# Kernel optimization log

Measured on AMD Instinct MI355X. Metric: run time of the kernel, lower is better.

Reference implementation:

```python
import jax, jax.numpy as jnp
import numpy as np

B, N, C = 4, 4096, 512
K = 683  # ceil(N / ratio=6.0)
TAU = 1.0
W_OCC, W_REP, W_ENT = 1.0, 0.1, 0.01
REP_TOPK, REP_MARGIN = 4, -1.0
NEG = -1e9


def setup_inputs() -> dict:
    key = jax.random.key(0)
    ks = jax.random.split(key, 5)
    s = jax.random.normal(ks[0], (B, N, C), jnp.float32)
    mu = jax.random.normal(ks[1], (B, N, 3), jnp.float32)
    # SPD covariance per residue: L L^T + 0.1 I
    L = jax.random.normal(ks[2], (B, N, 3, 3), jnp.float32) * 0.3
    Sigma = jnp.einsum('bnij,bnkj->bnik', L, L) + 0.1 * jnp.eye(3, dtype=jnp.float32)
    mask = jnp.ones((B, N), jnp.float32)
    W = jax.random.normal(ks[3], (C, C), jnp.float32) / np.sqrt(C).astype(np.float32)
    b = jnp.zeros((C,), jnp.float32)
    slots = jax.random.normal(ks[4], (K, C), jnp.float32) * 0.02
    return {"s": s, "mu": mu, "Sigma": Sigma, "mask": mask, "W": W, "b": b, "slots": slots}


def reference(s, mu, Sigma, mask, W, b, slots):
    Kk = slots.shape[0]
    # A = softmax((Linear(s)) . slots / tau), masked
    s_proj = jnp.einsum('bnc,dc->bnd', s, W) + b            # nn.Linear: x @ W^T + b
    logits = jnp.einsum('bnc,kc->bnk', s_proj, slots) / TAU
    logits = jnp.where((mask < 0.5)[..., None], NEG, logits)
    A = jax.nn.softmax(logits, axis=-1) * mask[..., None]   # [B,N,K]

    denom = jnp.maximum(A.sum(axis=1), 1e-8)                # [B,K]
    s_c = jnp.einsum('bnk,bnc->bkc', A, s) / denom[..., None]

    # moment-matching merge
    w = A / (A.sum(axis=1, keepdims=True) + 1e-8)           # [B,N,K]
    mu_c = jnp.einsum('bnk,bnd->bkd', w, mu)                # [B,K,3]
    intra = jnp.einsum('bnk,bnij->bkij', w, Sigma)          # [B,K,3,3]
    diff = mu[:, :, None, :] - mu_c[:, None, :, :]          # [B,N,K,3]
    inter = jnp.einsum('bnk,bnki,bnkj->bkij', w, diff, diff)
    Sigma_c = intra + inter                                 # [B,K,3,3]

    # occupancy balance loss
    occ = A.sum(axis=1)
    occ = occ / jnp.maximum(occ.sum(axis=-1, keepdims=True), 1e-8)
    loss_occ = jnp.mean((occ - 1.0 / Kk) ** 2)

    # repulsion loss (pairwise Gaussian overlap)
    delta = mu_c[:, :, None, :] - mu_c[:, None, :, :]       # [B,K,K,3]
    sig_sum = Sigma_c[:, :, None] + Sigma_c[:, None, :]     # [B,K,K,3,3]
    inv = jnp.linalg.inv(sig_sum + 1e-6 * jnp.eye(3, dtype=s.dtype))
    dist2 = jnp.einsum('bpqi,bpqij,bpqj->bpq', delta, inv, delta)
    score = -0.5 * dist2
    eye = jnp.eye(Kk, dtype=bool)[None]
    score = jnp.where(eye, NEG, score)
    top = jax.lax.top_k(score, min(REP_TOPK, Kk - 1))[0]
    loss_rep = jnp.mean(jax.nn.relu(top - REP_MARGIN))

    # entropy loss
    Ac = jnp.maximum(A, 1e-8)
    ent = -(Ac * jnp.log(Ac)).sum(axis=-1)                  # [B,N]
    loss_ent = (ent * mask).sum() / jnp.maximum(mask.sum(), 1.0)

    total = W_OCC * loss_occ + W_REP * loss_rep + W_ENT * loss_ent
    return (A, s_c, mu_c, Sigma_c, loss_occ, loss_rep, loss_ent, total)
```

## Files before the change

### kernel.cpp

```cpp
#include <hip/hip_runtime.h>
#include <math.h>

#define B_    4
#define N_    4096
#define C_    512
#define KSLOT 683

using bf16x8 = __attribute__((ext_vector_type(8))) short;
using f32x4  = __attribute__((ext_vector_type(4))) float;

#define OFF_A    0
#define OFF_SC   (B_*N_*KSLOT)
#define OFF_MU   (OFF_SC + B_*KSLOT*C_)
#define OFF_SIG  (OFF_MU + B_*KSLOT*3)
#define OFF_LOSS (OFF_SIG + B_*KSLOT*9)

#define WS_MOM    0
#define WS_INVMAX (WS_MOM + B_*KSLOT*16)
#define WS_OCCTB  (WS_INVMAX + B_*KSLOT)
#define WS_OCCT   (WS_OCCTB + 256)
#define WS_ENTB   (WS_OCCT + 4)
#define WS_MSB    (WS_ENTB + 256)
#define WS_OCCLB  (WS_MSB + 256)
#define WS_REPB   (WS_OCCLB + 256)
#define WS_BS     (WS_REPB + 256)
#define WS_FEND   (WS_BS + 704)

#define US_BASE  (WS_FEND*2)
#define US_SBF   US_BASE
#define US_STF   (US_SBF + B_*N_*C_)
#define US_WSL   (US_STF + B_*C_*N_)
#define US_FT    (US_WSL + 704*C_)
#define US_ATB   (US_FT + B_*16*N_)
#define US_END   (US_ATB + (size_t)B_*768*N_)


__device__ __forceinline__ ushort f2bf(float x) {
  union { float f; unsigned u; } v; v.f = x;
  unsigned r = v.u + 0x7fffu + ((v.u >> 16) & 1u);
  return (ushort)(r >> 16);
}

__device__ __forceinline__ float bf2f(ushort x) {
  union { unsigned u; float f; } v; v.u = ((unsigned)x) << 16;
  return v.f;
}

__device__ __forceinline__ float blockSum256(float v, float* red) {
#pragma unroll
  for (int off = 32; off; off >>= 1) v += __shfl_xor(v, off);
  __syncthreads();
  if ((threadIdx.x & 63) == 0) red[threadIdx.x >> 6] = v;
  __syncthreads();
  return red[0] + red[1] + red[2] + red[3];
}

__device__ __forceinline__ void top4_insert(float v, float& t0, float& t1, float& t2, float& t3) {
  if (v > t3) {
    if (v > t2) {
      t3 = t2;
      if (v > t1) {
        t2 = t1;
        if (v > t0) { t1 = t0; t0 = v; } else t1 = v;
      } else t2 = v;
    } else t3 = v;
  }
}

__global__ __launch_bounds__(256) void prep_all(const float* __restrict__ s,
                                                ushort* __restrict__ sbf,
                                                ushort* __restrict__ stf,
                                                const float* __restrict__ mu,
                                                const float* __restrict__ Sig,
                                                ushort* __restrict__ ftg,
                                                const float* __restrict__ slots,
                                                const float* __restrict__ W,
                                                ushort* __restrict__ wsl,
                                                const float* __restrict__ bvec,
                                                float* __restrict__ bs) {
  __shared__ __align__(16) char PS[16640];
  const int bid = blockIdx.x;
  const int t = threadIdx.x;
  if (bid < 342) {
    float (*SL)[512] = (float(*)[512])PS;
    const int idx = bid;
    const int k0 = (idx % 171) * 4;
    const int c = (idx / 171) * 256 + t;
    for (int id2 = t; id2 < 4 * 512; id2 += 256) {
      int kk = id2 >> 9, d = id2 & 511;
      SL[kk][d] = (k0 + kk < KSLOT) ? slots[(size_t)(k0 + kk) * C_ + d] : 0.f;
    }
    __syncthreads();
    float acc[4];
#pragma unroll
    for (int i = 0; i < 4; ++i) acc[i] = 0.f;
    for (int d0 = 0; d0 < C_; d0 += 8) {
      float wv[8];
#pragma unroll
      for (int j = 0; j < 8; ++j) wv[j] = W[(size_t)(d0 + j) * C_ + c];
#pragma unroll
      for (int j = 0; j < 8; ++j) {
#pragma unroll
        for (int i = 0; i < 4; ++i) acc[i] += SL[i][d0 + j] * wv[j];
      }
    }
#pragma unroll
    for (int i = 0; i < 4; ++i)
      if (k0 + i < KSLOT) wsl[(size_t)(k0 + i) * C_ + c] = f2bf(acc[i]);
  } else if (bid < 513) {
    const int widx = (bid - 342) * 4 + (t >> 6);
    const int lane = t & 63;
    if (widx < KSLOT) {
      const float* srow = slots + (size_t)widx * C_;
      float acc = 0.f;
#pragma unroll
      for (int j = 0; j < 8; ++j) {
        int d = lane + j * 64;
        acc += srow[d] * bvec[d];
      }
#pragma unroll
      for (int off = 32; off; off >>= 1) acc += __shfl_xor(acc, off);
      if (lane == 0) bs[widx] = acc;
    }
  } else if (bid < 577) {
    ushort (*FT)[272] = (ushort(*)[272])PS;
    const int fb = bid - 513;
    const size_t ng = (size_t)fb * 256 + t;
    const float* mp = mu + ng * 3;
    const float* sp = Sig + ng * 9;
    float m0 = mp[0], m1 = mp[1], m2 = mp[2];
    FT[0][t] = 0x3F80;
    FT[1][t] = f2bf(m0); FT[2][t] = f2bf(m1); FT[3][t] = f2bf(m2);
    FT[4][t] = f2bf(m0 * m0); FT[5][t] = f2bf(m0 * m1); FT[6][t] = f2bf(m0 * m2);
    FT[7][t] = f2bf(m1 * m1); FT[8][t] = f2bf(m1 * m2); FT[9][t] = f2bf(m2 * m2);
    FT[10][t] = f2bf(sp[0]); FT[11][t] = f2bf(sp[1]); FT[12][t] = f2bf(sp[2]);
    FT[13][t] = f2bf(sp[4]); FT[14][t] = f2bf(sp[5]); FT[15][t] = f2bf(sp[8]);
    __syncthreads();
    const int b = (int)((fb * 256) >> 12);
    const int n0b = (fb * 256) & (N_ - 1);
    for (int u = t; u < 512; u += 256) {
      int f = u >> 5, off = (u & 31) * 8;
      *(uint4*)(ftg + ((size_t)b * 16 + f) * N_ + n0b + off) = *(uint4*)(&FT[f][off]);
    }
  } else {
    float (*T)[65] = (float(*)[65])PS;
    const int cid = bid - 577;
    const int b = cid >> 9;
    const int rem = cid & 511;
    const int n0 = (rem >> 3) * 64;
    const int c0 = (rem & 7) * 64;
    const int tr = t >> 4;
    const int tc = (t & 15) * 4;
#pragma unroll
    for (int i = 0; i < 4; ++i) {
      const int row = i * 16 + tr;
      float4 v = *(const float4*)(s + ((size_t)(b * N_ + n0 + row)) * C_ + c0 + tc);
      ushort4 u;
      u.x = f2bf(v.x); u.y = f2bf(v.y); u.z = f2bf(v.z); u.w = f2bf(v.w);
      *(ushort4*)(sbf + ((size_t)(b * N_ + n0 + row)) * C_ + c0 + tc) = u;
      T[row][tc + 0] = v.x; T[row][tc + 1] = v.y;
      T[row][tc + 2] = v.z; T[row][tc + 3] = v.w;
    }
    __syncthreads();
#pragma unroll
    for (int i = 0; i < 4; ++i) {
      const int c = i * 16 + tr;
      const int n4 = tc;
      ushort4 o;
      o.x = f2bf(T[n4 + 0][c]); o.y = f2bf(T[n4 + 1][c]);
      o.z = f2bf(T[n4 + 2][c]); o.w = f2bf(T[n4 + 3][c]);
      *(ushort4*)(stf + ((size_t)(b * C_ + c0 + c)) * N_ + n0 + n4) = o;
    }
  }
}

__global__ __launch_bounds__(256) void bs_kernel(const float* __restrict__ slots,
                                                 const float* __restrict__ bvec,
                                                 float* __restrict__ bs) {
  int k = blockIdx.x * 256 + threadIdx.x;
  if (k >= KSLOT) return;
  const float* srow = slots + (size_t)k * C_;
  float acc = 0.f;
  for (int d = 0; d < C_; ++d) acc += srow[d] * bvec[d];
  bs[k] = acc;
}

__device__ __forceinline__ void g1_epilogue(
    f32x4 (&acc)[11], const int rowbase, const int t, const int lane,
    const int rowg, const int colw,
    const float* __restrict__ bs, const float* __restrict__ mask,
    float* __restrict__ Aout, ushort* __restrict__ atb,
    float* __restrict__ entb, float* __restrict__ msb,
    ushort* Af, float (&red4)[32][4], const int binid, const int nthreads) {
  __syncthreads();
  int cols[11]; bool valid[11];
#pragma unroll
  for (int cf = 0; cf < 11; ++cf) {
    cols[cf] = colw * 176 + cf * 16 + (lane & 15);
    valid[cf] = (cols[cf] < KSLOT);
    float bv = valid[cf] ? bs[cols[cf]] : 0.f;
#pragma unroll
    for (int r = 0; r < 4; ++r) acc[cf][r] += bv;
  }
  float m4[4];
#pragma unroll
  for (int r = 0; r < 4; ++r) m4[r] = -3.0e38f;
#pragma unroll
  for (int cf = 0; cf < 11; ++cf)
    if (valid[cf]) {
#pragma unroll
      for (int r = 0; r < 4; ++r) m4[r] = fmaxf(m4[r], acc[cf][r]);
    }
#pragma unroll
  for (int off = 1; off < 16; off <<= 1) {
#pragma unroll
    for (int r = 0; r < 4; ++r) m4[r] = fmaxf(m4[r], __shfl_xor(m4[r], off));
  }
  if ((lane & 15) == 0) {
#pragma unroll
    for (int r = 0; r < 4; ++r) red4[rowg * 16 + (lane >> 4) * 4 + r][colw] = m4[r];
  }
  __syncthreads();
#pragma unroll
  for (int r = 0; r < 4; ++r) {
    int rl = rowg * 16 + (lane >> 4) * 4 + r;
    m4[r] = fmaxf(fmaxf(red4[rl][0], red4[rl][1]), fmaxf(red4[rl][2], red4[rl][3]));
  }
  __syncthreads();
  float s4[4] = {0.f, 0.f, 0.f, 0.f};
#pragma unroll
  for (int cf = 0; cf < 11; ++cf)
    if (valid[cf]) {
#pragma unroll
      for (int r = 0; r < 4; ++r) {
        float e = __expf(acc[cf][r] - m4[r]);
        acc[cf][r] = e;
        s4[r] += e;
      }
    }
#pragma unroll
  for (int off = 1; off < 16; off <<= 1) {
#pragma unroll
    for (int r = 0; r < 4; ++r) s4[r] += __shfl_xor(s4[r], off);
  }
  if ((lane & 15) == 0) {
#pragma unroll
    for (int r = 0; r < 4; ++r) red4[rowg * 16 + (lane >> 4) * 4 + r][colw] = s4[r];
  }
  __syncthreads();
  float inv4[4], mr4[4];
#pragma unroll
  for (int r = 0; r < 4; ++r) {
    int rl = rowg * 16 + (lane >> 4) * 4 + r;
    float S = red4[rl][0] + red4[rl][1] + red4[rl][2] + red4[rl][3];
    inv4[r] = 1.f / S;
    mr4[r] = mask[rowbase + rl];
  }
  __syncthreads();
  float ent4[4] = {0.f, 0.f, 0.f, 0.f};
#pragma unroll
  for (int cf = 0; cf < 11; ++cf)
    if (valid[cf]) {
#pragma unroll
      for (int r = 0; r < 4; ++r) {
        int rl = rowg * 16 + (lane >> 4) * 4 + r;
        float a = acc[cf][r] * inv4[r] * mr4[r];
        Af[rl * KSLOT + cols[cf]] = f2bf(a);
        float ac = fmaxf(a, 1e-8f);
        ent4[r] -= ac * __logf(ac);
      }
    }
#pragma unroll
  for (int off = 1; off < 16; off <<= 1) {
#pragma unroll
    for (int r = 0; r < 4; ++r) ent4[r] += __shfl_xor(ent4[r], off);
  }
  if ((lane & 15) == 0) {
#pragma unroll
    for (int r = 0; r < 4; ++r) red4[rowg * 16 + (lane >> 4) * 4 + r][colw] = ent4[r];
  }
  __syncthreads();
  if (t < 64) {
    float er = 0.f, ms = 0.f;
    if (t < 32) {
      float e = red4[t][0] + red4[t][1] + red4[t][2] + red4[t][3];
      float m = mask[rowbase + t];
      er = e * m; ms = m;
    }
#pragma unroll
    for (int off = 32; off; off >>= 1) { er += __shfl_xor(er, off); ms += __shfl_xor(ms, off); }
    if (t == 0) {
      atomicAdd(&entb[binid], er);
      atomicAdd(&msb[binid], ms);
    }
  }
  float* Ag = Aout + (size_t)rowbase * KSLOT;
  for (int i = t; i < (32 * KSLOT) / 4; i += nthreads) {
    ushort4 u4 = *(const ushort4*)(Af + i * 4);
    float4 v;
    v.x = bf2f(u4.x); v.y = bf2f(u4.y); v.z = bf2f(u4.z); v.w = bf2f(u4.w);
    *(float4*)(Ag + i * 4) = v;
  }
  {
    const int bb = rowbase >> 12;
    const int n0b = rowbase & (N_ - 1);
    ushort* Atb = atb + ((size_t)bb * 768) * N_ + n0b;
    for (int u = t; u < KSLOT * 4; u += nthreads) {
      int k = u >> 2, q = u & 3;
      ushort tmp[8];
#pragma unroll
      for (int j = 0; j < 8; ++j) tmp[j] = Af[(q * 8 + j) * KSLOT + k];
      *(uint4*)(Atb + (size_t)k * N_ + q * 8) = *(uint4*)tmp;
    }
  }
}

__global__ __launch_bounds__(512)
void gemm1sm(const ushort* __restrict__ sbf,
             const ushort* __restrict__ wsl,
             const float* __restrict__ bs,
             const float* __restrict__ mask,
             float* __restrict__ Aout,
             ushort* __restrict__ atb,
             float* __restrict__ entb,
             float* __restrict__ msb) {
  __shared__ __align__(16) char SMEM[49152];
  __shared__ float red4[32][4];
  const int t = threadIdx.x;
  const int lane = t & 63;
  const int w = t >> 6;
  const int rowg = w >> 2;
  const int colw = w & 3;
  const int row0 = blockIdx.x * 32;
  const int r16 = rowg * 16 + (lane & 15);

  const ushort* arow = sbf + (size_t)(row0 + r16) * C_ + (lane >> 4) * 8;
  bf16x8 g0 = *(const bf16x8*)(arow);
  bf16x8 p0;

  f32x4 acc[11];
  f32x4 zero = {0.f, 0.f, 0.f, 0.f};
#pragma unroll
  for (int cf = 0; cf < 11; ++cf) acc[cf] = zero;

  const int ach = (lane >> 4);
#pragma unroll
  for (int slab = 0; slab < 16; ++slab) {
    if (slab) __syncthreads();
#pragma unroll
    for (int i = 0; i < 6; ++i) {
      int idx = t + i * 512;
      int r = idx >> 2;
      int chs = (idx & 3) ^ (r & 3);
      const ushort* g = wsl + (size_t)r * C_ + slab * 32 + chs * 8;
      char* l = (char*)SMEM + (t & 448) * 16 + i * 8192;
      __builtin_amdgcn_global_load_lds(
          (const __attribute__((address_space(1))) void*)g,
          (__attribute__((address_space(3))) void*)l, 16, 0, 0);
    }
    __syncthreads();
    if (slab < 15) p0 = *(const bf16x8*)(arow + (slab + 1) * 32);
#pragma unroll
    for (int cf = 0; cf < 11; ++cf) {
      int br = colw * 176 + cf * 16 + (lane & 15);
      bf16x8 bf = *(const bf16x8*)(SMEM + br * 64 + ((ach * 16) ^ ((br & 3) << 4)));
      acc[cf] = __builtin_amdgcn_mfma_f32_16x16x32_bf16(g0, bf, acc[cf], 0, 0, 0);
    }
    g0 = p0;
  }

  ushort* Af = (ushort*)SMEM;
  g1_epilogue(acc, row0, t, lane, rowg, colw, bs, mask, Aout, atb, entb, msb,
              Af, red4, blockIdx.x & 255, 512);
}

#define G2BUFB 18432
__global__ __launch_bounds__(256) void gemm2t(const ushort* __restrict__ atb,
                                              const ushort* __restrict__ stf,
                                              const ushort* __restrict__ ftg,
                                              float* __restrict__ sc,
                                              float* __restrict__ MOM) {
  __shared__ __align__(16) char LB[2 * G2BUFB];
  const int t = threadIdx.x;
  const int lane = t & 63;
  const int w = t >> 6;
  const int wm = w >> 1;
  const int wn = w & 1;
  const int fhw = blockIdx.x;
  const int logical = (fhw & 7) * 44 + (fhw >> 3);
  const int kt = logical % 11;
  const int ct = (logical / 11) & 7;
  const int b  = logical / 88;
  const bool do_mom = (ct == 0);
  const ushort* Ab = atb + ((size_t)b * 768 + kt * 64) * N_;
  const ushort* Sb = stf + ((size_t)b * C_ + ct * 64) * N_;
  const ushort* Fb = ftg + ((size_t)b * 16) * N_;

  f32x4 zero = {0.f, 0.f, 0.f, 0.f};
  f32x4 acc[2][2];
#pragma unroll
  for (int i = 0; i < 2; ++i)
#pragma unroll
    for (int j = 0; j < 2; ++j) acc[i][j] = zero;
  f32x4 accf[2];
#pragma unroll
  for (int i = 0; i < 2; ++i) accf[i] = zero;

#define G2_STAGE(BUFI, NB)                                                   \
  {                                                                          \
    char* AtL = LB + (BUFI) * G2BUFB;                                        \
    char* SsL = AtL + 8192;                                                  \
    char* FtL = AtL + 16384;                                                 \
    _Pragma("unroll")                                                        \
    for (int i = 0; i < 2; ++i) {                                            \
      int idx = t + i * 256;                                                 \
      int r = idx >> 3;                                                      \
      int chs = (idx & 7) ^ (r & 7);                                         \
      const ushort* g = Ab + (size_t)r * N_ + (NB) + chs * 8;                \
      char* l = AtL + i * 4096 + (t & 192) * 16;                             \
      __builtin_amdgcn_global_load_lds(                                      \
          (const __attribute__((address_space(1))) void*)g,                  \
          (__attribute__((address_space(3))) void*)l, 16, 0, 0);             \
    }                                                                        \
    _Pragma("unroll")                                                        \
    for (int i = 0; i < 2; ++i) {                                            \
      int idx = t + i * 256;                                                 \
      int r = idx >> 3;                                                      \
      int chs = (idx & 7) ^ (r & 7);                                         \
      const ushort* g = Sb + (size_t)r * N_ + (NB) + chs * 8;                \
      char* l = SsL + i * 4096 + (t & 192) * 16;                             \
      __builtin_amdgcn_global_load_lds(                                      \
          (const __attribute__((address_space(1))) void*)g,                  \
          (__attribute__((address_space(3))) void*)l, 16, 0, 0);             \
    }                                                                        \
    if (do_mom && t < 128) {                                                 \
      int idx = t;                                                           \
      int r = idx >> 3;                                                      \
      int chs = (idx & 7) ^ (r & 7);                                         \
      const ushort* g = Fb + (size_t)r * N_ + (NB) + chs * 8;                \
      char* l = FtL + (t & 192) * 16;                                       \
      __builtin_amdgcn_global_load_lds(                                      \
          (const __attribute__((address_space(1))) void*)g,                  \
          (__attribute__((address_space(3))) void*)l, 16, 0, 0);             \
    }                                                                        \
  }

  G2_STAGE(0, 0)
  for (int st = 0; st < 64; ++st) {
    const int cur = st & 1;
    __syncthreads();
    if (st < 63) G2_STAGE(cur ^ 1, (st + 1) * 64)
    char* AtL = LB + cur * G2BUFB;
    char* SsL = AtL + 8192;
    char* FtL = AtL + 16384;
#pragma unroll
    for (int ks2 = 0; ks2 < 2; ++ks2) {
      const int ach = ks2 * 4 + (lane >> 4);
      bf16x8 afr[2], bfr[2];
#pragma unroll
      for (int kf = 0; kf < 2; ++kf) {
        int ar = wm * 32 + kf * 16 + (lane & 15);
        afr[kf] = *(const bf16x8*)(AtL + ar * 128 + ((ach * 16) ^ ((ar & 7) << 4)));
      }
#pragma unroll
      for (int cg = 0; cg < 2; ++cg) {
        int br = wn * 32 + cg * 16 + (lane & 15);
        bfr[cg] = *(const bf16x8*)(SsL + br * 128 + ((ach * 16) ^ ((br & 7) << 4)));
      }
#pragma unroll
      for (int kf = 0; kf < 2; ++kf)
#pragma unroll
        for (int cg = 0; cg < 2; ++cg)
          acc[kf][cg] = __builtin_amdgcn_mfma_f32_16x16x32_bf16(afr[kf], bfr[cg], acc[kf][cg], 0, 0, 0);
      if (do_mom && wn == 0) {
        int fr = lane & 15;
        bf16x8 ffr = *(const bf16x8*)(FtL + fr * 128 + ((ach * 16) ^ ((fr & 7) << 4)));
#pragma unroll
        for (int kf = 0; kf < 2; ++kf)
          accf[kf] = __builtin_amdgcn_mfma_f32_16x16x32_bf16(afr[kf], ffr, accf[kf], 0, 0, 0);
      }
    }
  }
#undef G2_STAGE

#pragma unroll
  for (int kf = 0; kf < 2; ++kf) {
#pragma unroll
    for (int r = 0; r < 4; ++r) {
      int k = kt * 64 + wm * 32 + kf * 16 + (lane >> 4) * 4 + r;
      if (k >= KSLOT) continue;
      float* dst = sc + ((size_t)(b * KSLOT + k)) * C_ + ct * 64 + wn * 32;
#pragma unroll
      for (int cg = 0; cg < 2; ++cg)
        dst[cg * 16 + (lane & 15)] = acc[kf][cg][r];
    }
  }
  if (do_mom && wn == 0) {
#pragma unroll
    for (int kf = 0; kf < 2; ++kf) {
#pragma unroll
      for (int r = 0; r < 4; ++r) {
        int k = kt * 64 + wm * 32 + kf * 16 + (lane >> 4) * 4 + r;
        if (k >= KSLOT) continue;
        MOM[((size_t)b * KSLOT + k) * 16 + (lane & 15)] = accf[kf][r];
      }
    }
  }
}

__global__ __launch_bounds__(128) void scale_sc(float* __restrict__ sc,
                                                const float* __restrict__ invmax) {
  const int bk = blockIdx.x;
  const float sv = invmax[bk];
  float4* p = (float4*)(sc + (size_t)bk * C_);
  int t = threadIdx.x;
  float4 v = p[t];
  v.x *= sv; v.y *= sv; v.z *= sv; v.w *= sv;
  p[t] = v;
}

__global__ __launch_bounds__(256) void moments_kernel(const float* __restrict__ Amat,
                                                      const float* __restrict__ mu,
                                                      const float* __restrict__ Sig,
                                                      float* __restrict__ MOM) {
  __shared__ float red[64][17];
  const int b = blockIdx.z;
  const int kx = threadIdx.x & 63;
  const int k = blockIdx.x * 64 + kx;
  const int ng = threadIdx.x >> 6;
  const int n0 = blockIdx.y * 128;
  const bool valid = (k < KSLOT);

  float acc[16];
#pragma unroll
  for (int i = 0; i < 16; ++i) acc[i] = 0.f;

  const float* Abase = Amat + (size_t)b * N_ * KSLOT + k;
  const float* mubase = mu + ((size_t)b * N_) * 3;
  const float* sgbase = Sig + ((size_t)b * N_) * 9;

  for (int j = 0; j < 32; ++j) {
    const int n = n0 + ng + j * 4;
    float a = valid ? Abase[(size_t)n * KSLOT] : 0.f;
    const float* mp = mubase + (size_t)n * 3;
    const float* sp = sgbase + (size_t)n * 9;
    float m0 = mp[0], m1 = mp[1], m2 = mp[2];
    acc[0] += a;
    acc[1] += a * m0; acc[2] += a * m1; acc[3] += a * m2;
    acc[4] += a * m0 * m0; acc[5] += a * m0 * m1; acc[6] += a * m0 * m2;
    acc[7] += a * m1 * m1; acc[8] += a * m1 * m2; acc[9] += a * m2 * m2;
    acc[10] += a * sp[0]; acc[11] += a * sp[1]; acc[12] += a * sp[2];
    acc[13] += a * sp[4]; acc[14] += a * sp[5]; acc[15] += a * sp[8];
  }

  if (ng == 0) {
#pragma unroll
    for (int i = 0; i < 16; ++i) red[kx][i] = acc[i];
  }
  __syncthreads();
  if (ng == 1) {
#pragma unroll
    for (int i = 0; i < 16; ++i) red[kx][i] += acc[i];
  }
  __syncthreads();
  if (ng == 2) {
#pragma unroll
    for (int i = 0; i < 16; ++i) red[kx][i] += acc[i];
  }
  __syncthreads();
  if (ng == 3) {
#pragma unroll
    for (int i = 0; i < 16; ++i) red[kx][i] += acc[i];
  }
  __syncthreads();
  if (ng == 0 && valid) {
    float* dst = MOM + ((size_t)b * KSLOT + k) * 16;
#pragma unroll
    for (int i = 0; i < 16; ++i) atomicAdd(&dst[i], red[kx][i]);
  }
}

__global__ __launch_bounds__(256) void finalize_bk(const float* __restrict__ MOM,
                                                   float* __restrict__ muc,
                                                   float* __restrict__ sigc,
                                                   float* __restrict__ invmax,
                                                   float* __restrict__ occtb) {
  int bk = blockIdx.x * 256 + threadIdx.x;
  if (bk >= B_ * KSLOT) return;
  int b = bk / KSLOT;
  const float* T = MOM + (size_t)bk * 16;
  float den = T[0];
  float inv_eps = 1.f / (den + 1e-8f);
  float inv_mx = 1.f / fmaxf(den, 1e-8f);
  float mc0 = T[1] * inv_eps, mc1 = T[2] * inv_eps, mc2 = T[3] * inv_eps;
  float M0 = den * inv_eps;
  float cf = 2.f - M0;
  float S00 = (T[10] + T[4]) * inv_eps - cf * mc0 * mc0;
  float S01 = (T[11] + T[5]) * inv_eps - cf * mc0 * mc1;
  float S02 = (T[12] + T[6]) * inv_eps - cf * mc0 * mc2;
  float S11 = (T[13] + T[7]) * inv_eps - cf * mc1 * mc1;
  float S12 = (T[14] + T[8]) * inv_eps - cf * mc1 * mc2;
  float S22 = (T[15] + T[9]) * inv_eps - cf * mc2 * mc2;
  muc[(size_t)bk * 3 + 0] = mc0;
  muc[(size_t)bk * 3 + 1] = mc1;
  muc[(size_t)bk * 3 + 2] = mc2;
  float* sg = sigc + (size_t)bk * 9;
  sg[0] = S00; sg[1] = S01; sg[2] = S02;
  sg[3] = S01; sg[4] = S11; sg[5] = S12;
  sg[6] = S02; sg[7] = S12; sg[8] = S22;
  invmax[bk] = inv_mx;
  atomicAdd(&occtb[b * 64 + (threadIdx.x & 63)], den);
}

__global__ __launch_bounds__(256) void occ_loss_kernel(const float* __restrict__ MOM,
                                                       const float* __restrict__ occtb,
                                                       float* __restrict__ occlb) {
  __shared__ float red[4];
  __shared__ float occT[4];
  int tid = threadIdx.x;
  {
    float v = occtb[tid];
#pragma unroll
    for (int off = 32; off; off >>= 1) v += __shfl_xor(v, off);
    if ((tid & 63) == 0) occT[tid >> 6] = v;
  }
  __syncthreads();
  int bk = blockIdx.x * 256 + tid;
  float d2 = 0.f;
  if (bk < B_ * KSLOT) {
    int b = bk / KSLOT;
    float den = MOM[(size_t)bk * 16];
    float occ = den / fmaxf(occT[b], 1e-8f);
    float d = occ - (1.f / (float)KSLOT);
    d2 = d * d;
  }
  float ssum = blockSum256(d2, red);
  if (tid == 0) occlb[blockIdx.x] = ssum;
}

__global__ __launch_bounds__(256) void repulsion_kernel2(const float* __restrict__ muc,
                                                         const float* __restrict__ sigc,
                                                         float* __restrict__ repb) {
  __shared__ float L[KSLOT * 13];
  const int b = blockIdx.y;
  const int t = threadIdx.x;
  const float* mb = muc + (size_t)b * KSLOT * 3;
  const float* sb = sigc + (size_t)b * KSLOT * 9;
  for (int idx = t; idx < KSLOT * 3; idx += 256) {
    int r = idx / 3, c = idx - r * 3;
    L[r * 13 + c] = mb[idx];
  }
  for (int idx = t; idx < KSLOT * 9; idx += 256) {
    int r = idx / 9, c = idx - r * 9;
    L[r * 13 + 3 + c] = sb[idx];
  }
  __syncthreads();
  const int w = t >> 6, lane = t & 63;
  const int p = blockIdx.x * 4 + w;
  if (p >= KSLOT) return;
  const float* Lp = L + p * 13;
  const float mp0 = Lp[0], mp1 = Lp[1], mp2 = Lp[2];
  const float pa = Lp[3], pb = Lp[4], pc = Lp[5], pd = Lp[7], pe = Lp[8], pf = Lp[11];
  float t0 = -3e38f, t1 = -3e38f, t2 = -3e38f, t3 = -3e38f;
  for (int q = lane; q < KSLOT; q += 64) {
    if (q == p) continue;
    const float* Lq = L + q * 13;
    float d0 = mp0 - Lq[0];
    float d1 = mp1 - Lq[1];
    float d2 = mp2 - Lq[2];
    float a  = pa + Lq[3] + 1e-6f;
    float bb = pb + Lq[4];
    float cc = pc + Lq[5];
    float d  = pd + Lq[7] + 1e-6f;
    float e  = pe + Lq[8];
    float f  = pf + Lq[11] + 1e-6f;
    float C00 = d * f - e * e;
    float C01 = cc * e - bb * f;
    float C02 = bb * e - cc * d;
    float C11 = a * f - cc * cc;
    float C12 = bb * cc - a * e;
    float C22 = a * d - bb * bb;
    float det = a * C00 + bb * C01 + cc * C02;
    float dist2 = (C00 * d0 * d0 + C11 * d1 * d1 + C22 * d2 * d2 +
                   2.f * (C01 * d0 * d1 + C02 * d0 * d2 + C12 * d1 * d2)) / det;
    top4_insert(-0.5f * dist2, t0, t1, t2, t3);
  }
#pragma unroll
  for (int off = 1; off < 64; off <<= 1) {
    float u0 = __shfl_xor(t0, off);
    float u1 = __shfl_xor(t1, off);
    float u2 = __shfl_xor(t2, off);
    float u3 = __shfl_xor(t3, off);
    top4_insert(u0, t0, t1, t2, t3);
    top4_insert(u1, t0, t1, t2, t3);
    top4_insert(u2, t0, t1, t2, t3);
    top4_insert(u3, t0, t1, t2, t3);
  }
  if (lane == 0) {
    float s = fmaxf(t0 + 1.f, 0.f) + fmaxf(t1 + 1.f, 0.f) +
              fmaxf(t2 + 1.f, 0.f) + fmaxf(t3 + 1.f, 0.f);
    atomicAdd(&repb[(b * KSLOT + p) & 255], s);
  }
}

__global__ __launch_bounds__(256) void final_scalars(const float* __restrict__ entb,
                                                     const float* __restrict__ msb,
                                                     const float* __restrict__ occlb,
                                                     const float* __restrict__ repb,
                                                     float* __restrict__ out) {
  __shared__ float red[4];
  int tid = threadIdx.x;
  float e = blockSum256(entb[tid], red);
  float ms = blockSum256(msb[tid], red);
  float oc = blockSum256(occlb[tid], red);
  float rp = blockSum256(repb[tid], red);
  if (tid == 0) {
    float loss_ent = e / fmaxf(ms, 1.f);
    float loss_occ = oc / (float)(B_ * KSLOT);
    float loss_rep = rp / (float)(B_ * KSLOT * 4);
    out[0] = loss_occ;
    out[1] = loss_rep;
    out[2] = loss_ent;
    out[3] = 1.0f * loss_occ + 0.1f * loss_rep + 0.01f * loss_ent;
  }
}


__global__ __launch_bounds__(256) void wslots_kernel(const float* __restrict__ slots,
                                                     const float* __restrict__ W,
                                                     float* __restrict__ Wsl) {
  int k = blockIdx.x;
  int c = blockIdx.y * 256 + threadIdx.x;
  const float* srow = slots + (size_t)k * C_;
  float acc = 0.f;
  for (int d = 0; d < C_; d += 4) {
    acc += srow[d] * W[(size_t)d * C_ + c];
    acc += srow[d + 1] * W[(size_t)(d + 1) * C_ + c];
    acc += srow[d + 2] * W[(size_t)(d + 2) * C_ + c];
    acc += srow[d + 3] * W[(size_t)(d + 3) * C_ + c];
  }
  Wsl[(size_t)k * C_ + c] = acc;
}

__global__ __launch_bounds__(256) void softmax_rows(float* __restrict__ Amat,
                                                    const float* __restrict__ mask,
                                                    float* __restrict__ entb,
                                                    float* __restrict__ msb) {
  __shared__ float red[4];
  const int row = blockIdx.x;
  const int tid = threadIdx.x;
  float* rowp = Amat + (size_t)row * KSLOT;
  const float m = mask[row];
  const bool msk = (m < 0.5f);
  float v[3];
#pragma unroll
  for (int i = 0; i < 3; ++i) {
    int k = tid + i * 256;
    if (k < KSLOT) {
      float l = rowp[k];
      v[i] = msk ? -1e9f : l;
    } else v[i] = -3.0e38f;
  }
  float lmax = fmaxf(fmaxf(v[0], v[1]), v[2]);
#pragma unroll
  for (int off = 32; off; off >>= 1) lmax = fmaxf(lmax, __shfl_xor(lmax, off));
  __syncthreads();
  if ((tid & 63) == 0) red[tid >> 6] = lmax;
  __syncthreads();
  lmax = fmaxf(fmaxf(red[0], red[1]), fmaxf(red[2], red[3]));
  float lsum = 0.f;
#pragma unroll
  for (int i = 0; i < 3; ++i) {
    int k = tid + i * 256;
    float e = (k < KSLOT) ? expf(v[i] - lmax) : 0.f;
    v[i] = e;
    lsum += e;
  }
  lsum = blockSum256(lsum, red);
  float inv = 1.f / lsum;
  float ent = 0.f;
#pragma unroll
  for (int i = 0; i < 3; ++i) {
    int k = tid + i * 256;
    if (k < KSLOT) {
      float a = v[i] * inv * m;
      rowp[k] = a;
      float ac = fmaxf(a, 1e-8f);
      ent -= ac * logf(ac);
    }
  }
  ent = blockSum256(ent, red);
  if (tid == 0) {
    int bin = blockIdx.x & 255;
    atomicAdd(&entb[bin], ent * m);
    atomicAdd(&msb[bin], m);
  }
}

__global__ __launch_bounds__(256) void gemm_nt(const float* __restrict__ Am,
                                               const float* __restrict__ Bm,
                                               const float* __restrict__ bias,
                                               float* __restrict__ Cm,
                                               int M, int Nout, int Kd,
                                               int lda, int ldb, int ldc) {
  __shared__ float As[16][132];
  __shared__ float Bs[16][132];
  const int tid = threadIdx.x;
  const int tx = tid & 15, ty = tid >> 4;
  const int m0 = blockIdx.x * 128, n0 = blockIdx.y * 128;
  float acc[8][8];
#pragma unroll
  for (int i = 0; i < 8; ++i)
#pragma unroll
    for (int j = 0; j < 8; ++j) acc[i][j] = 0.f;
  const int r = tid >> 1, hc = (tid & 1) * 8;
  for (int k0 = 0; k0 < Kd; k0 += 16) {
    float va[8], vb[8];
    int gm = m0 + r;
    if (gm < M) {
      const float* p = Am + (size_t)gm * lda + k0 + hc;
      *(float4*)(va) = *(const float4*)(p);
      *(float4*)(va + 4) = *(const float4*)(p + 4);
    } else {
#pragma unroll
      for (int i = 0; i < 8; ++i) va[i] = 0.f;
    }
    int gn = n0 + r;
    if (gn < Nout) {
      const float* p = Bm + (size_t)gn * ldb + k0 + hc;
      *(float4*)(vb) = *(const float4*)(p);
      *(float4*)(vb + 4) = *(const float4*)(p + 4);
    } else {
#pragma unroll
      for (int i = 0; i < 8; ++i) vb[i] = 0.f;
    }
#pragma unroll
    for (int i = 0; i < 8; ++i) As[hc + i][r] = va[i];
#pragma unroll
    for (int i = 0; i < 8; ++i) Bs[hc + i][r] = vb[i];
    __syncthreads();
#pragma unroll
    for (int kk = 0; kk < 16; ++kk) {
      float a[8], bb[8];
      *(float4*)(a) = *(const float4*)&As[kk][ty * 8];
      *(float4*)(a + 4) = *(const float4*)&As[kk][ty * 8 + 4];
      *(float4*)(bb) = *(const float4*)&Bs[kk][tx * 8];
      *(float4*)(bb + 4) = *(const float4*)&Bs[kk][tx * 8 + 4];
#pragma unroll
      for (int i = 0; i < 8; ++i)
#pragma unroll
        for (int j = 0; j < 8; ++j) acc[i][j] += a[i] * bb[j];
    }
    __syncthreads();
  }
#pragma unroll
  for (int i = 0; i < 8; ++i) {
    int gm = m0 + ty * 8 + i;
    if (gm >= M) continue;
    float* crow = Cm + (size_t)gm * ldc;
#pragma unroll
    for (int j = 0; j < 8; ++j) {
      int gn = n0 + tx * 8 + j;
      if (gn < Nout) crow[gn] = acc[i][j] + bias[gn];
    }
  }
}

__global__ __launch_bounds__(256) void gemm_tn(const float* __restrict__ Aall,
                                               const float* __restrict__ Ball,
                                               const float* __restrict__ scale,
                                               float* __restrict__ Call) {
  const int b = blockIdx.z;
  const float* Am = Aall + (size_t)b * N_ * KSLOT;
  const float* Bv = Ball + (size_t)b * N_ * C_;
  float* Cm = Call + (size_t)b * KSLOT * C_;
  const float* sc = scale + (size_t)b * KSLOT;
  __shared__ float As[16][132];
  __shared__ float Bs[16][68];
  const int tid = threadIdx.x;
  const int tx = tid & 15, ty = tid >> 4;
  const int m0 = blockIdx.x * 128, n0 = blockIdx.y * 64;
  float acc[8][4];
#pragma unroll
  for (int i = 0; i < 8; ++i)
#pragma unroll
    for (int j = 0; j < 4; ++j) acc[i][j] = 0.f;
  const int rr = tid >> 4;
  const int mq = tid & 15;
  const int cq = (tid & 15) * 4;
  for (int r0 = 0; r0 < N_; r0 += 16) {
#pragma unroll
    for (int i = 0; i < 8; ++i) {
      int mm = mq + 16 * i;
      int gm = m0 + mm;
      As[rr][mm] = (gm < KSLOT) ? Am[(size_t)(r0 + rr) * KSLOT + gm] : 0.f;
    }
    *(float4*)&Bs[rr][cq] = *(const float4*)(Bv + (size_t)(r0 + rr) * C_ + n0 + cq);
    __syncthreads();
#pragma unroll
    for (int kk = 0; kk < 16; ++kk) {
      float a[8], bb[4];
      *(float4*)(a) = *(const float4*)&As[kk][ty * 8];
      *(float4*)(a + 4) = *(const float4*)&As[kk][ty * 8 + 4];
      *(float4*)(bb) = *(const float4*)&Bs[kk][tx * 4];
#pragma unroll
      for (int i = 0; i < 8; ++i)
#pragma unroll
        for (int j = 0; j < 4; ++j) acc[i][j] += a[i] * bb[j];
    }
    __syncthreads();
  }
#pragma unroll
  for (int i = 0; i < 8; ++i) {
    int gm = m0 + ty * 8 + i;
    if (gm < KSLOT) {
      float s = sc[gm];
      float4 v;
      v.x = acc[i][0] * s; v.y = acc[i][1] * s; v.z = acc[i][2] * s; v.w = acc[i][3] * s;
      *(float4*)(Cm + (size_t)gm * C_ + n0 + tx * 4) = v;
    }
  }
}

extern "C" void kernel_launch(void* const* d_in, const int* in_sizes, int n_in,
                              void* d_out, int out_size, void* d_ws, size_t ws_size,
                              hipStream_t stream) {
  const float* s     = (const float*)d_in[0];
  const float* mu    = (const float*)d_in[1];
  const float* Sig   = (const float*)d_in[2];
  const float* mask  = (const float*)d_in[3];
  const float* W     = (const float*)d_in[4];
  const float* bvec  = (const float*)d_in[5];
  const float* slots = (const float*)d_in[6];
  float* out = (float*)d_out;
  float* ws  = (float*)d_ws;

  float* Amat = out + OFF_A;
  const bool fast = (ws_size >= (size_t)US_END * 2 + 64);

  (void)hipMemsetAsync(ws, 0, WS_FEND * sizeof(float), stream);

  if (fast) {
    ushort* usw = (ushort*)ws;
    ushort* sbf = usw + US_SBF;
    ushort* stf = usw + US_STF;
    ushort* wsl = usw + US_WSL;
    ushort* ftg = usw + US_FT;
    ushort* atb = usw + US_ATB;

    prep_all<<<dim3(2625), 256, 0, stream>>>(
        s, sbf, stf, mu, Sig, ftg, slots, W, wsl, bvec, ws + WS_BS);

    gemm1sm<<<dim3(B_ * N_ / 32), 512, 0, stream>>>(
        sbf, wsl, ws + WS_BS, mask, Amat, atb, ws + WS_ENTB, ws + WS_MSB);

    gemm2t<<<dim3(352), 256, 0, stream>>>(
        atb, stf, ftg, out + OFF_SC, ws + WS_MOM);

    finalize_bk<<<dim3((B_ * KSLOT + 255) / 256), 256, 0, stream>>>(
        ws + WS_MOM, out + OFF_MU, out + OFF_SIG, ws + WS_INVMAX, ws + WS_OCCTB);

    occ_loss_kernel<<<dim3((B_ * KSLOT + 255) / 256), 256, 0, stream>>>(
        ws + WS_MOM, ws + WS_OCCTB, ws + WS_OCCLB);

    scale_sc<<<dim3(B_ * KSLOT), 128, 0, stream>>>(out + OFF_SC, ws + WS_INVMAX);

    repulsion_kernel2<<<dim3((KSLOT + 3) / 4, B_), 256, 0, stream>>>(
        out + OFF_MU, out + OFF_SIG, ws + WS_REPB);

    final_scalars<<<dim3(1), 256, 0, stream>>>(
        ws + WS_ENTB, ws + WS_MSB, ws + WS_OCCLB, ws + WS_REPB, out + OFF_LOSS);
  } else {
    float* Wsl = out + OFF_SC;

    bs_kernel<<<dim3(3), 256, 0, stream>>>(slots, bvec, ws + WS_BS);
    wslots_kernel<<<dim3(KSLOT, 2), 256, 0, stream>>>(slots, W, Wsl);
    gemm_nt<<<dim3((B_ * N_) / 128, (KSLOT + 127) / 128), 256, 0, stream>>>(
        s, Wsl, ws + WS_BS, Amat, B_ * N_, KSLOT, C_, C_, C_, KSLOT);
    softmax_rows<<<dim3(B_ * N_), 256, 0, stream>>>(Amat, mask, ws + WS_ENTB, ws + WS_MSB);
    moments_kernel<<<dim3(11, N_ / 128, B_), 256, 0, stream>>>(
        Amat, mu, Sig, ws + WS_MOM);
    finalize_bk<<<dim3((B_ * KSLOT + 255) / 256), 256, 0, stream>>>(
        ws + WS_MOM, out + OFF_MU, out + OFF_SIG, ws + WS_INVMAX, ws + WS_OCCTB);
    occ_loss_kernel<<<dim3((B_ * KSLOT + 255) / 256), 256, 0, stream>>>(
        ws + WS_MOM, ws + WS_OCCTB, ws + WS_OCCLB);
    gemm_tn<<<dim3((KSLOT + 127) / 128, C_ / 64, B_), 256, 0, stream>>>(
        Amat, s, ws + WS_INVMAX, out + OFF_SC);
    repulsion_kernel2<<<dim3((KSLOT + 3) / 4, B_), 256, 0, stream>>>(
        out + OFF_MU, out + OFF_SIG, ws + WS_REPB);
    final_scalars<<<dim3(1), 256, 0, stream>>>(
        ws + WS_ENTB, ws + WS_MSB, ws + WS_OCCLB, ws + WS_REPB, out + OFF_LOSS);
  }
}
```

Measured before the change: 163.5 us.

## Compute column sums in gemm1 epilogue and fuse s_c scaling into gemm2

The gemm1 softmax epilogue now accumulates per-slot column sums of A and atomically adds them into a new workspace denominator buffer. A tiny inv_den kernel turns these into reciprocals before gemm2, which then scales s_c as it writes it out, so the separate scale_sc read-modify-write pass over s_c is gone. This adds per-block atomics and one small launch, and the denominator now sums fp32 A values, whereas finalize_bk may still derive its own invmax from the moments.

```diff
diff --git a/kernel.cpp b/kernel.cpp
--- a/kernel.cpp
+++ b/kernel.cpp
@@ -24,7 +24,8 @@
 #define WS_OCCLB  (WS_MSB + 256)
 #define WS_REPB   (WS_OCCLB + 256)
 #define WS_BS     (WS_REPB + 256)
-#define WS_FEND   (WS_BS + 704)
+#define WS_DEN    (WS_BS + 704)
+#define WS_FEND   (WS_DEN + B_*KSLOT)
 
 #define US_BASE  (WS_FEND*2)
 #define US_SBF   US_BASE
@@ -191,6 +192,7 @@
     const float* __restrict__ bs, const float* __restrict__ mask,
     float* __restrict__ Aout, ushort* __restrict__ atb,
     float* __restrict__ entb, float* __restrict__ msb,
+    float* __restrict__ denb,
     ushort* Af, float (&red4)[32][4], const int binid, const int nthreads) {
   __syncthreads();
   int cols[11]; bool valid[11];
@@ -258,6 +260,9 @@
   }
   __syncthreads();
   float ent4[4] = {0.f, 0.f, 0.f, 0.f};
+  float csum[11];
+#pragma unroll
+  for (int cf = 0; cf < 11; ++cf) csum[cf] = 0.f;
 #pragma unroll
   for (int cf = 0; cf < 11; ++cf)
     if (valid[cf]) {
@@ -268,6 +273,7 @@
         Af[rl * KSLOT + cols[cf]] = f2bf(a);
         float ac = fmaxf(a, 1e-8f);
         ent4[r] -= ac * __logf(ac);
+        csum[cf] += a;
       }
     }
 #pragma unroll
@@ -293,6 +299,14 @@
       atomicAdd(&entb[binid], er);
       atomicAdd(&msb[binid], ms);
     }
+  }
+#pragma unroll
+  for (int cf = 0; cf < 11; ++cf) {
+    float v = csum[cf];
+    v += __shfl_xor(v, 16);
+    v += __shfl_xor(v, 32);
+    if ((lane & 63) < 16 && valid[cf])
+      atomicAdd(&denb[cols[cf]], v);
   }
   float* Ag = Aout + (size_t)rowbase * KSLOT;
   for (int i = t; i < (32 * KSLOT) / 4; i += nthreads) {
@@ -323,7 +337,8 @@
              float* __restrict__ Aout,
              ushort* __restrict__ atb,
              float* __restrict__ entb,
-             float* __restrict__ msb) {
+             float* __restrict__ msb,
+             float* __restrict__ den) {
   __shared__ __align__(16) char SMEM[49152];
   __shared__ float red4[32][4];
   const int t = threadIdx.x;
@@ -370,14 +385,22 @@
   }
 
   ushort* Af = (ushort*)SMEM;
+  const int bb = row0 >> 12;
   g1_epilogue(acc, row0, t, lane, rowg, colw, bs, mask, Aout, atb, entb, msb,
-              Af, red4, blockIdx.x & 255, 512);
+              den + bb * KSLOT, Af, red4, blockIdx.x & 255, 512);
+}
+
+__global__ __launch_bounds__(256) void inv_den(const float* __restrict__ den,
+                                               float* __restrict__ invmax) {
+  int bk = blockIdx.x * 256 + threadIdx.x;
+  if (bk < B_ * KSLOT) invmax[bk] = 1.f / fmaxf(den[bk], 1e-8f);
 }
 
 #define G2BUFB 18432
 __global__ __launch_bounds__(256) void gemm2t(const ushort* __restrict__ atb,
                                               const ushort* __restrict__ stf,
                                               const ushort* __restrict__ ftg,
+                                              const float* __restrict__ invmax,
                                               float* __restrict__ sc,
                                               float* __restrict__ MOM) {
   __shared__ __align__(16) char LB[2 * G2BUFB];
@@ -489,10 +512,11 @@
     for (int r = 0; r < 4; ++r) {
       int k = kt * 64 + wm * 32 + kf * 16 + (lane >> 4) * 4 + r;
       if (k >= KSLOT) continue;
+      float sv = invmax[b * KSLOT + k];
       float* dst = sc + ((size_t)(b * KSLOT + k)) * C_ + ct * 64 + wn * 32;
 #pragma unroll
       for (int cg = 0; cg < 2; ++cg)
-        dst[cg * 16 + (lane & 15)] = acc[kf][cg][r];
+        dst[cg * 16 + (lane & 15)] = acc[kf][cg][r] * sv;
     }
   }
   if (do_mom && wn == 0) {
@@ -506,17 +530,6 @@
       }
     }
   }
-}
-
-__global__ __launch_bounds__(128) void scale_sc(float* __restrict__ sc,
-                                                const float* __restrict__ invmax) {
-  const int bk = blockIdx.x;
-  const float sv = invmax[bk];
-  float4* p = (float4*)(sc + (size_t)bk * C_);
-  int t = threadIdx.x;
-  float4 v = p[t];
-  v.x *= sv; v.y *= sv; v.z *= sv; v.w *= sv;
-  p[t] = v;
 }
 
 __global__ __launch_bounds__(256) void moments_kernel(const float* __restrict__ Amat,
@@ -952,18 +965,19 @@
         s, sbf, stf, mu, Sig, ftg, slots, W, wsl, bvec, ws + WS_BS);
 
     gemm1sm<<<dim3(B_ * N_ / 32), 512, 0, stream>>>(
-        sbf, wsl, ws + WS_BS, mask, Amat, atb, ws + WS_ENTB, ws + WS_MSB);
+        sbf, wsl, ws + WS_BS, mask, Amat, atb, ws + WS_ENTB, ws + WS_MSB, ws + WS_DEN);
+
+    inv_den<<<dim3((B_ * KSLOT + 255) / 256), 256, 0, stream>>>(
+        ws + WS_DEN, ws + WS_INVMAX);
 
     gemm2t<<<dim3(352), 256, 0, stream>>>(
-        atb, stf, ftg, out + OFF_SC, ws + WS_MOM);
+        atb, stf, ftg, ws + WS_INVMAX, out + OFF_SC, ws + WS_MOM);
 
     finalize_bk<<<dim3((B_ * KSLOT + 255) / 256), 256, 0, stream>>>(
         ws + WS_MOM, out + OFF_MU, out + OFF_SIG, ws + WS_INVMAX, ws + WS_OCCTB);
 
     occ_loss_kernel<<<dim3((B_ * KSLOT + 255) / 256), 256, 0, stream>>>(
         ws + WS_MOM, ws + WS_OCCTB, ws + WS_OCCLB);
-
-    scale_sc<<<dim3(B_ * KSLOT), 128, 0, stream>>>(out + OFF_SC, ws + WS_INVMAX);
 
     repulsion_kernel2<<<dim3((KSLOT + 3) / 4, B_), 256, 0, stream>>>(
         out + OFF_MU, out + OFF_SIG, ws + WS_REPB);
```

Result: slower. 196.5 us (+20.2%).
